# Optimization experiments

Hardware: AMD Instinct MI355X
Metric: run time of the kernel (lower is better)

The kernel has to match this reference:

```python
import jax, jax.numpy as jnp
import numpy as np

IN_FEATURES = 4096
OUT_FEATURES = 4096
RANK = 1024
BATCH, SEQ = 4, 2048


def setup_inputs() -> dict:
    key = jax.random.key(0)
    k_x, k_u, k_s, k_v, k_b = jax.random.split(key, 5)
    # Factors of the SVD-decomposed weight. In the original module these come
    # from torch.svd of a trained weight; here random factors preserve the math.
    x = jax.random.normal(k_x, (BATCH, SEQ, IN_FEATURES), dtype=jnp.float32)
    U = jax.random.normal(k_u, (OUT_FEATURES, RANK), dtype=jnp.float32) / np.sqrt(OUT_FEATURES)
    S = jnp.abs(jax.random.normal(k_s, (RANK,), dtype=jnp.float32)) + 0.1  # singular values > 0
    Vt = jax.random.normal(k_v, (IN_FEATURES, RANK), dtype=jnp.float32) / np.sqrt(IN_FEATURES)
    bias = jax.random.normal(k_b, (OUT_FEATURES,), dtype=jnp.float32) * 0.02
    return {"x": x, "U": U, "S": S, "Vt": Vt, "bias": bias}


def reference(x, U, S, Vt, bias):
    # Original: weight = U @ diag(S) @ Vt.T  (shape [out, in]);
    #           y = F.linear(x, weight, bias) = x @ weight.T + bias
    # Algebraically identical low-rank path (never materializes [out, in]):
    #   y = ((x @ Vt) * S) @ U.T + bias
    h = jnp.einsum('bsi,ir->bsr', x, Vt) * S       # [B, S, rank]
    y = jnp.einsum('bsr,or->bso', h, U) + bias     # [B, S, out]
    return y
```

## Files before the change

kernel.cpp:

```cpp
#include <hip/hip_runtime.h>

#define M_DIM 8192
#define IN_F  4096
#define RANK_ 1024
#define OUT_F 4096

typedef __bf16 bf16x8 __attribute__((ext_vector_type(8)));
typedef float  f32x4  __attribute__((ext_vector_type(4)));
typedef unsigned short ushort8 __attribute__((ext_vector_type(8)));

__device__ __forceinline__ unsigned short f2bf(float f) {
    unsigned int u = __float_as_uint(f);
    u += 0x7FFFu + ((u >> 16) & 1u);
    return (unsigned short)(u >> 16);
}

__global__ void cvt_f32_bf16(const float* __restrict__ in,
                             unsigned short* __restrict__ out, int n8) {
    int stride = gridDim.x * blockDim.x;
    for (int i = blockIdx.x * blockDim.x + threadIdx.x; i < n8; i += stride) {
        const float4* p = (const float4*)in + (size_t)i * 2;
        float4 a = p[0];
        float4 b = p[1];
        ushort8 o;
        o[0] = f2bf(a.x); o[1] = f2bf(a.y); o[2] = f2bf(a.z); o[3] = f2bf(a.w);
        o[4] = f2bf(b.x); o[5] = f2bf(b.y); o[6] = f2bf(b.z); o[7] = f2bf(b.w);
        ((ushort8*)out)[i] = o;
    }
}

__global__ void transpose_scale(const float* __restrict__ vt,
                                const float* __restrict__ S,
                                unsigned short* __restrict__ out) {
    __shared__ float tile[32][33];
    const int kb = blockIdx.x * 32;
    const int rb = blockIdx.y * 32;
    const int tx = threadIdx.x & 31;
    const int ty = threadIdx.x >> 5;
    #pragma unroll
    for (int j = 0; j < 32; j += 8)
        tile[ty + j][tx] = vt[(size_t)(kb + ty + j) * RANK_ + rb + tx];
    __syncthreads();
    #pragma unroll
    for (int j = 0; j < 32; j += 8) {
        int r = rb + ty + j;
        float s = S[r];
        out[(size_t)r * IN_F + kb + tx] = f2bf(tile[tx][ty + j] * s);
    }
}

template<int EPI>
__global__ __launch_bounds__(256, 2)
void gemm_bt(const unsigned short* __restrict__ A,
             const unsigned short* __restrict__ B,
             void* __restrict__ Cv,
             const float* __restrict__ bias,
             int N, int K) {
    __shared__ unsigned short sA[128 * 64];
    __shared__ unsigned short sB[128 * 64];

    const int l  = threadIdx.x & 63;
    const int w  = threadIdx.x >> 6;
    const int wr = w >> 1, wc = w & 1;
    const int col0 = blockIdx.x * 128;
    const int row0 = blockIdx.y * 128;

    const unsigned short* gA = A + (size_t)row0 * K;
    const unsigned short* gB = B + (size_t)col0 * K;

    f32x4 acc[4][4];
    const f32x4 z = {0.f, 0.f, 0.f, 0.f};
    #pragma unroll
    for (int i = 0; i < 4; ++i)
        #pragma unroll
        for (int j = 0; j < 4; ++j) acc[i][j] = z;

    auto stage = [&](const unsigned short* __restrict__ g,
                     unsigned short* __restrict__ s, int k0) {
        #pragma unroll
        for (int i = 0; i < 4; ++i) {
            int chunk = (i * 4 + w) * 64 + l;
            int r  = chunk >> 3;
            int c  = chunk & 7;
            int cs = c ^ (r & 7);
            const unsigned short* src = g + (size_t)r * K + k0 + cs * 8;
            __builtin_amdgcn_global_load_lds(
                (const __attribute__((address_space(1))) void*)src,
                (__attribute__((address_space(3))) void*)(s + chunk * 8),
                16, 0, 0);
        }
    };

    stage(gA, sA, 0);
    stage(gB, sB, 0);

    const int nK = K >> 6;
    for (int kt = 0; kt < nK; ++kt) {
        __syncthreads();
        #pragma unroll
        for (int kk = 0; kk < 2; ++kk) {
            bf16x8 av[4], bv[4];
            #pragma unroll
            for (int mi = 0; mi < 4; ++mi) {
                int r = wr * 64 + mi * 16 + (l & 15);
                int c = (kk * 4 + (l >> 4)) ^ (r & 7);
                av[mi] = *(const bf16x8*)((const char*)sA + r * 128 + c * 16);
            }
            #pragma unroll
            for (int nj = 0; nj < 4; ++nj) {
                int r = wc * 64 + nj * 16 + (l & 15);
                int c = (kk * 4 + (l >> 4)) ^ (r & 7);
                bv[nj] = *(const bf16x8*)((const char*)sB + r * 128 + c * 16);
            }
            #pragma unroll
            for (int mi = 0; mi < 4; ++mi)
                #pragma unroll
                for (int nj = 0; nj < 4; ++nj)
                    acc[mi][nj] = __builtin_amdgcn_mfma_f32_16x16x32_bf16(
                        av[mi], bv[nj], acc[mi][nj], 0, 0, 0);
        }
        if (kt + 1 < nK) {
            __syncthreads();
            stage(gA, sA, (kt + 1) << 6);
            stage(gB, sB, (kt + 1) << 6);
        }
    }

    const int cr = (l >> 4) << 2;
    const int cc = l & 15;
    const int mB = row0 + wr * 64;
    const int nB = col0 + wc * 64;
    if (EPI == 0) {
        unsigned short* C = (unsigned short*)Cv;
        #pragma unroll
        for (int mi = 0; mi < 4; ++mi)
            #pragma unroll
            for (int nj = 0; nj < 4; ++nj) {
                size_t base = (size_t)(mB + mi * 16 + cr) * N + (nB + nj * 16 + cc);
                #pragma unroll
                for (int r = 0; r < 4; ++r)
                    C[base + (size_t)r * N] = f2bf(acc[mi][nj][r]);
            }
    } else {
        float* C = (float*)Cv;
        #pragma unroll
        for (int nj = 0; nj < 4; ++nj) {
            float bvv = bias[nB + nj * 16 + cc];
            #pragma unroll
            for (int mi = 0; mi < 4; ++mi) {
                size_t base = (size_t)(mB + mi * 16 + cr) * N + (nB + nj * 16 + cc);
                #pragma unroll
                for (int r = 0; r < 4; ++r)
                    C[base + (size_t)r * N] = acc[mi][nj][r] + bvv;
            }
        }
    }
}

extern "C" void kernel_launch(void* const* d_in, const int* in_sizes, int n_in,
                              void* d_out, int out_size, void* d_ws, size_t ws_size,
                              hipStream_t stream) {
    const float* x    = (const float*)d_in[0];
    const float* U    = (const float*)d_in[1];
    const float* S    = (const float*)d_in[2];
    const float* Vt   = (const float*)d_in[3];
    const float* bias = (const float*)d_in[4];

    unsigned short* xb  = (unsigned short*)d_ws;
    unsigned short* vtT = xb  + (size_t)M_DIM * IN_F;
    unsigned short* ub  = vtT + (size_t)RANK_ * IN_F;
    unsigned short* h   = ub  + (size_t)OUT_F * RANK_;

    hipLaunchKernelGGL(cvt_f32_bf16, dim3(2048), dim3(256), 0, stream,
                       x, xb, (M_DIM * IN_F) / 8);
    hipLaunchKernelGGL(cvt_f32_bf16, dim3(512), dim3(256), 0, stream,
                       U, ub, (OUT_F * RANK_) / 8);
    hipLaunchKernelGGL(transpose_scale, dim3(IN_F / 32, RANK_ / 32), dim3(256), 0, stream,
                       Vt, S, vtT);

    hipLaunchKernelGGL((gemm_bt<0>), dim3(RANK_ / 128, M_DIM / 128), dim3(256), 0, stream,
                       xb, vtT, (void*)h, (const float*)nullptr, RANK_, IN_F);
    hipLaunchKernelGGL((gemm_bt<1>), dim3(OUT_F / 128, M_DIM / 128), dim3(256), 0, stream,
                       h, ub, d_out, bias, OUT_F, RANK_);
}
```

Before: 406.7 us.

## Rewrite GEMMs as 8-wave double-buffered kernels with larger tiles

Replaces the single-buffered 128x128 GEMM with a 512-thread kernel using 256x128 and 256x256 tiles, double-buffered LDS with prefetch two k-steps ahead and explicit vmcnt waits. It splits each k-step into quadrants separated by barriers with s_setprio around the MFMA bursts, and remaps block IDs across XCDs. The goal is to hide global load latency behind MFMA work and raise arithmetic intensity per block. In exchange the kernel uses more LDS and registers per block, which can lower occupancy, and the hand-written waitcnt counts must match the number of loads issued per stage.

New measurement: 451.4 us. 11.0% more time.

```diff
diff --git a/kernel.cpp b/kernel.cpp
--- a/kernel.cpp
+++ b/kernel.cpp
@@ -49,37 +49,44 @@
     }
 }
 
-template<int EPI>
-__global__ __launch_bounds__(256, 2)
-void gemm_bt(const unsigned short* __restrict__ A,
-             const unsigned short* __restrict__ B,
-             void* __restrict__ Cv,
-             const float* __restrict__ bias,
-             int N, int K) {
-    __shared__ unsigned short sA[128 * 64];
-    __shared__ unsigned short sB[128 * 64];
-
-    const int l  = threadIdx.x & 63;
-    const int w  = threadIdx.x >> 6;
-    const int wr = w >> 1, wc = w & 1;
-    const int col0 = blockIdx.x * 128;
-    const int row0 = blockIdx.y * 128;
+template<int BM, int BN, int EPI>
+__global__ __launch_bounds__(512, 2)
+void gemm8p(const unsigned short* __restrict__ A,
+            const unsigned short* __restrict__ B,
+            void* __restrict__ Cv,
+            const float* __restrict__ bias,
+            int N, int K, int nbx) {
+    constexpr int LA = BM / 64;
+    constexpr int LB = BN / 64;
+    constexpr int L  = LA + LB;
+    constexpr int NF = BN / 4 / 16;
+    constexpr int NH = NF / 2 > 0 ? NF / 2 : 1;
+
+    __shared__ unsigned short sA[2][BM * 64];
+    __shared__ unsigned short sB[2][BN * 64];
+
+    const int tid = threadIdx.x;
+    const int l = tid & 63;
+    const int w = tid >> 6;
+    const int wr = w >> 2;
+    const int wc = w & 3;
+
+    const int nwg = gridDim.x;
+    const int bid = blockIdx.x;
+    const int wg  = (bid & 7) * (nwg >> 3) + (bid >> 3);
+    const int bx  = wg % nbx;
+    const int by  = wg / nbx;
+    const int row0 = by * BM;
+    const int col0 = bx * BN;
 
     const unsigned short* gA = A + (size_t)row0 * K;
     const unsigned short* gB = B + (size_t)col0 * K;
 
-    f32x4 acc[4][4];
-    const f32x4 z = {0.f, 0.f, 0.f, 0.f};
-    #pragma unroll
-    for (int i = 0; i < 4; ++i)
-        #pragma unroll
-        for (int j = 0; j < 4; ++j) acc[i][j] = z;
-
     auto stage = [&](const unsigned short* __restrict__ g,
-                     unsigned short* __restrict__ s, int k0) {
-        #pragma unroll
-        for (int i = 0; i < 4; ++i) {
-            int chunk = (i * 4 + w) * 64 + l;
+                     unsigned short* __restrict__ s, int k0, int nload) {
+        #pragma unroll 4
+        for (int i = 0; i < nload; ++i) {
+            int chunk = i * 512 + tid;
             int r  = chunk >> 3;
             int c  = chunk & 7;
             int cs = c ^ (r & 7);
@@ -91,51 +98,88 @@
         }
     };
 
-    stage(gA, sA, 0);
-    stage(gB, sB, 0);
-
-    const int nK = K >> 6;
-    for (int kt = 0; kt < nK; ++kt) {
-        __syncthreads();
-        #pragma unroll
-        for (int kk = 0; kk < 2; ++kk) {
-            bf16x8 av[4], bv[4];
-            #pragma unroll
-            for (int mi = 0; mi < 4; ++mi) {
-                int r = wr * 64 + mi * 16 + (l & 15);
-                int c = (kk * 4 + (l >> 4)) ^ (r & 7);
-                av[mi] = *(const bf16x8*)((const char*)sA + r * 128 + c * 16);
+    f32x4 acc[8][NF];
+    const f32x4 z = {0.f, 0.f, 0.f, 0.f};
+    #pragma unroll
+    for (int i = 0; i < 8; ++i)
+        #pragma unroll
+        for (int j = 0; j < NF; ++j) acc[i][j] = z;
+
+    const int nt = K >> 6;
+
+    stage(gA, sA[0], 0, LA);
+    stage(gB, sB[0], 0, LB);
+    stage(gA, sA[1], 64, LA);
+    stage(gB, sB[1], 64, LB);
+    if constexpr (L == 8) asm volatile("s_waitcnt vmcnt(8)" ::: "memory");
+    else                  asm volatile("s_waitcnt vmcnt(6)" ::: "memory");
+    __builtin_amdgcn_s_barrier();
+
+    int c = 0;
+    for (int t = 0; t < nt; ++t) {
+        const unsigned short* a_ = sA[c];
+        const unsigned short* b_ = sB[c];
+        bf16x8 av[4][2];
+        #pragma unroll
+        for (int q = 0; q < 4; ++q) {
+            const int mh = q >> 1, nh = q & 1;
+            if (nh == 0) {
+                #pragma unroll
+                for (int mi = 0; mi < 4; ++mi)
+                    #pragma unroll
+                    for (int ks = 0; ks < 2; ++ks) {
+                        int r  = wr * 128 + mh * 64 + mi * 16 + (l & 15);
+                        int ch = (ks * 4 + (l >> 4)) ^ (r & 7);
+                        av[mi][ks] = *(const bf16x8*)((const char*)a_ + r * 128 + ch * 16);
+                    }
             }
-            #pragma unroll
-            for (int nj = 0; nj < 4; ++nj) {
-                int r = wc * 64 + nj * 16 + (l & 15);
-                int c = (kk * 4 + (l >> 4)) ^ (r & 7);
-                bv[nj] = *(const bf16x8*)((const char*)sB + r * 128 + c * 16);
-            }
+            bf16x8 bv[NH][2];
+            #pragma unroll
+            for (int nj = 0; nj < NH; ++nj)
+                #pragma unroll
+                for (int ks = 0; ks < 2; ++ks) {
+                    int r  = wc * (NF * 16) + nh * (NH * 16) + nj * 16 + (l & 15);
+                    int ch = (ks * 4 + (l >> 4)) ^ (r & 7);
+                    bv[nj][ks] = *(const bf16x8*)((const char*)b_ + r * 128 + ch * 16);
+                }
+            __builtin_amdgcn_s_barrier();
+            __builtin_amdgcn_s_setprio(1);
             #pragma unroll
             for (int mi = 0; mi < 4; ++mi)
                 #pragma unroll
-                for (int nj = 0; nj < 4; ++nj)
-                    acc[mi][nj] = __builtin_amdgcn_mfma_f32_16x16x32_bf16(
-                        av[mi], bv[nj], acc[mi][nj], 0, 0, 0);
-        }
-        if (kt + 1 < nK) {
-            __syncthreads();
-            stage(gA, sA, (kt + 1) << 6);
-            stage(gB, sB, (kt + 1) << 6);
-        }
+                for (int nj = 0; nj < NH; ++nj)
+                    #pragma unroll
+                    for (int ks = 0; ks < 2; ++ks)
+                        acc[mh * 4 + mi][nh * NH + nj] =
+                            __builtin_amdgcn_mfma_f32_16x16x32_bf16(
+                                av[mi][ks], bv[nj][ks],
+                                acc[mh * 4 + mi][nh * NH + nj], 0, 0, 0);
+            __builtin_amdgcn_s_setprio(0);
+            __builtin_amdgcn_s_barrier();
+        }
+        if (t + 2 < nt) {
+            stage(gA, sA[c], (t + 2) << 6, LA);
+            stage(gB, sB[c], (t + 2) << 6, LB);
+            if constexpr (L == 8) asm volatile("s_waitcnt vmcnt(8)" ::: "memory");
+            else                  asm volatile("s_waitcnt vmcnt(6)" ::: "memory");
+            __builtin_amdgcn_s_barrier();
+        } else if (t + 1 < nt) {
+            asm volatile("s_waitcnt vmcnt(0)" ::: "memory");
+            __builtin_amdgcn_s_barrier();
+        }
+        c ^= 1;
     }
 
     const int cr = (l >> 4) << 2;
     const int cc = l & 15;
-    const int mB = row0 + wr * 64;
-    const int nB = col0 + wc * 64;
+    const int mB = row0 + wr * 128;
+    const int nB = col0 + wc * (NF * 16);
     if (EPI == 0) {
         unsigned short* C = (unsigned short*)Cv;
         #pragma unroll
-        for (int mi = 0; mi < 4; ++mi)
-            #pragma unroll
-            for (int nj = 0; nj < 4; ++nj) {
+        for (int mi = 0; mi < 8; ++mi)
+            #pragma unroll
+            for (int nj = 0; nj < NF; ++nj) {
                 size_t base = (size_t)(mB + mi * 16 + cr) * N + (nB + nj * 16 + cc);
                 #pragma unroll
                 for (int r = 0; r < 4; ++r)
@@ -144,10 +188,10 @@
     } else {
         float* C = (float*)Cv;
         #pragma unroll
-        for (int nj = 0; nj < 4; ++nj) {
+        for (int nj = 0; nj < NF; ++nj) {
             float bvv = bias[nB + nj * 16 + cc];
             #pragma unroll
-            for (int mi = 0; mi < 4; ++mi) {
+            for (int mi = 0; mi < 8; ++mi) {
                 size_t base = (size_t)(mB + mi * 16 + cr) * N + (nB + nj * 16 + cc);
                 #pragma unroll
                 for (int r = 0; r < 4; ++r)
@@ -178,8 +222,11 @@
     hipLaunchKernelGGL(transpose_scale, dim3(IN_F / 32, RANK_ / 32), dim3(256), 0, stream,
                        Vt, S, vtT);
 
-    hipLaunchKernelGGL((gemm_bt<0>), dim3(RANK_ / 128, M_DIM / 128), dim3(256), 0, stream,
-                       xb, vtT, (void*)h, (const float*)nullptr, RANK_, IN_F);
-    hipLaunchKernelGGL((gemm_bt<1>), dim3(OUT_F / 128, M_DIM / 128), dim3(256), 0, stream,
-                       h, ub, d_out, bias, OUT_F, RANK_);
-}
+    hipLaunchKernelGGL((gemm8p<256, 128, 0>),
+                       dim3((RANK_ / 128) * (M_DIM / 256)), dim3(512), 0, stream,
+                       xb, vtT, (void*)h, (const float*)nullptr,
+                       RANK_, IN_F, RANK_ / 128);
+    hipLaunchKernelGGL((gemm8p<256, 256, 1>),
+                       dim3((OUT_F / 256) * (M_DIM / 256)), dim3(512), 0, stream,
+                       h, ub, d_out, bias, OUT_F, RANK_, OUT_F / 256);
+}
```
